# Kernel optimization log

Hardware: AMD Instinct MI355X
Metric: run time of the kernel (lower is better)

Reference implementation:

```python
import jax, jax.numpy as jnp
import numpy as np

B, S, E, H = 4, 2048, 1024, 16
D = E // H  # d_k = 64
NEG = -1000000000.0  # matches torch masked_fill constant


def setup_inputs() -> dict:
    rk = jax.random.key(0)
    kq, kk, kv, km = jax.random.split(rk, 4)
    query = jax.random.normal(kq, (B, S, E), dtype=jnp.float32)
    key = jax.random.normal(kk, (B, S, E), dtype=jnp.float32)
    value = jax.random.normal(kv, (B, S, E), dtype=jnp.float32)
    mask = jax.random.randint(km, (B, S, S), 0, 2, dtype=jnp.int32)
    return {"query": query, "key": key, "value": value, "mask": mask}


def _split_heads(x):
    # (B, S, E) -> (B, H, S, D)
    return x.reshape(B, S, H, D).transpose(0, 2, 1, 3)


def reference(query, key, value, mask):
    q = _split_heads(query)
    k = _split_heads(key)
    v = _split_heads(value)
    scale = np.float32(1.0 / np.sqrt(D))
    scores = jnp.einsum('bhqd,bhkd->bhqk', q, k) * scale  # (B,H,S,S)
    scores = jnp.where(mask[:, None, :, :] == 0, jnp.float32(NEG), scores)
    weights = jax.nn.softmax(scores, axis=-1)
    attn = jnp.einsum('bhqk,bhkd->bhqd', weights, v)  # (B,H,S,D)
    concat = attn.transpose(0, 2, 1, 3).reshape(B, S, E)
    return concat
```

## Files before the change

kernel.cpp:

```cpp
#include <hip/hip_runtime.h>
#include <hip/hip_bf16.h>
#include <math.h>

constexpr int B = 4, S = 2048, E = 1024, H = 16, D = 64;
constexpr float NEGF = -1000000000.0f;
constexpr float KSCALE = 0.125f * 1.44269504f;

typedef __attribute__((ext_vector_type(8))) short short8;
typedef __attribute__((ext_vector_type(16))) float f32x16;

__device__ inline unsigned pk2(float a, float b) {
    unsigned ua = __builtin_bit_cast(unsigned, a) + 0x8000u;
    unsigned ub = __builtin_bit_cast(unsigned, b) + 0x8000u;
    return __builtin_amdgcn_perm(ub, ua, 0x07060302u);
}
__device__ inline void gl_lds16(const void* g, void* l) {
    __builtin_amdgcn_global_load_lds(
        (const __attribute__((address_space(1))) unsigned int*)g,
        (__attribute__((address_space(3))) unsigned int*)l, 16, 0, 0);
}

constexpr size_t WS_K  = 0;
constexpr size_t WS_VT = 18874368;
constexpr size_t WS_MB = 37748736;
constexpr size_t WS_NEED = 54525952;

__global__ void prep_all(const float* __restrict__ K, const float* __restrict__ V,
                         const int* __restrict__ M, char* __restrict__ ws) {
    __shared__ float Vf[64][69];
    const int bid = blockIdx.x, tid = threadIdx.x;

    {
        int g = bid * 256 + tid;
        int rowd = g >> 2, qtr = g & 3;
        int b = rowd >> 15, h = (rowd >> 11) & 15, s = rowd & 2047;
        const float* p = K + ((size_t)(b * S + s)) * E + h * 64 + qtr * 16;
        float4 v0 = *(const float4*)(p + 0),  v1 = *(const float4*)(p + 4);
        float4 v2 = *(const float4*)(p + 8),  v3 = *(const float4*)(p + 12);
        uint4 o0, o1;
        o0.x = pk2(v0.x * KSCALE, v0.y * KSCALE); o0.y = pk2(v0.z * KSCALE, v0.w * KSCALE);
        o0.z = pk2(v1.x * KSCALE, v1.y * KSCALE); o0.w = pk2(v1.z * KSCALE, v1.w * KSCALE);
        o1.x = pk2(v2.x * KSCALE, v2.y * KSCALE); o1.y = pk2(v2.z * KSCALE, v2.w * KSCALE);
        o1.z = pk2(v3.x * KSCALE, v3.y * KSCALE); o1.w = pk2(v3.z * KSCALE, v3.w * KSCALE);
        char* d = ws + WS_K + (size_t)rowd * 144 + qtr * 32;
        *(uint4*)d = o0; *(uint4*)(d + 16) = o1;
        if (qtr == 3) {
            uint4 z; z.x = z.y = z.z = z.w = 0;
            *(uint4*)(d + 32) = z;
        }
    }

    {
        int bh = bid >> 5, kt = bid & 31;
        int b = bh >> 4, h = bh & 15;
        {
            int r = tid >> 2, c4 = (tid & 3) * 16;
            const float* p = V + ((size_t)(b * S + kt * 64 + r)) * E + h * 64 + c4;
            float4 a = *(const float4*)(p + 0), bb = *(const float4*)(p + 4);
            float4 c = *(const float4*)(p + 8), dd = *(const float4*)(p + 12);
            *(float4*)&Vf[r][c4 + 0] = a;  *(float4*)&Vf[r][c4 + 4] = bb;
            *(float4*)&Vf[r][c4 + 8] = c;  *(float4*)&Vf[r][c4 + 12] = dd;
        }
        __syncthreads();
        int d = tid >> 2, sq = (tid & 3) * 16;
        float v[16];
#pragma unroll
        for (int i = 0; i < 16; ++i) v[i] = Vf[sq + i][d];
        uint4 o0, o1;
        o0.x = pk2(v[0], v[1]);   o0.y = pk2(v[2], v[3]);
        o0.z = pk2(v[4], v[5]);   o0.w = pk2(v[6], v[7]);
        o1.x = pk2(v[8], v[9]);   o1.y = pk2(v[10], v[11]);
        o1.z = pk2(v[12], v[13]); o1.w = pk2(v[14], v[15]);
        char* o = ws + WS_VT + ((size_t)(bh * 32 + kt)) * 9216 + d * 144 + sq * 2;
        *(uint4*)o = o0; *(uint4*)(o + 16) = o1;
        if (sq == 48) {
            uint4 z; z.x = z.y = z.z = z.w = 0;
            *(uint4*)(o + 32) = z;
        }
    }

    {
        unsigned* Mb = (unsigned*)(ws + WS_MB);
        const int t = bid * 256 + tid;
#pragma unroll
        for (int it = 0; it < 8; ++it) {
            int gidx = it * 524288 + t;
            int4 mv = *((const int4*)M + gidx);
            unsigned d = (mv.x ? 0xFFu : 0u) | (mv.y ? 0xFF00u : 0u)
                       | (mv.z ? 0xFF0000u : 0u) | (mv.w ? 0xFF000000u : 0u);
            int row = gidx >> 4, g = gidx & 15;
            Mb[row * 16 + (g & 1) * 8 + (g >> 1)] = d;
        }
    }
}

__global__ __launch_bounds__(256, 2)
void fa_mfma(const float* __restrict__ Q, const char* __restrict__ ws,
             float* __restrict__ O) {
    __shared__ char smem[55296];
    const int tid = threadIdx.x;
    const int w = tid >> 6, lane = tid & 63;
    const int L5 = lane & 31, h6 = lane >> 5;
    const int h = blockIdx.x & 15, b = (blockIdx.x >> 4) & 3, qt = blockIdx.x >> 6;
    const int bh = b * 16 + h;
    const int q0w = qt * 256 + w * 64;
    char* const Ps = smem + 18432 + w * 9216;

    const char* Kws  = ws + WS_K;
    const char* Vtws = ws + WS_VT;
    const int qA = q0w + L5, qB = qA + 32;
    const char* mrowA = ws + WS_MB + ((size_t)(b * S + qA)) * 2048 + h6 * 32;
    const char* mrowB = ws + WS_MB + ((size_t)(b * S + qB)) * 2048 + h6 * 32;

    short8 qf[2][4];
#pragma unroll
    for (int nb = 0; nb < 2; ++nb)
#pragma unroll
        for (int ks = 0; ks < 4; ++ks) {
            const float* qp = Q + ((size_t)(b * S + q0w + nb * 32 + L5)) * E
                                + h * 64 + ks * 16 + h6 * 8;
            float4 a = *(const float4*)qp;
            float4 c = *(const float4*)(qp + 4);
            uint4 u;
            u.x = pk2(a.x, a.y); u.y = pk2(a.z, a.w);
            u.z = pk2(c.x, c.y); u.w = pk2(c.z, c.w);
            qf[nb][ks] = *(short8*)&u;
        }

    f32x16 acc[2][2];
#pragma unroll
    for (int mb = 0; mb < 2; ++mb)
#pragma unroll
        for (int nb = 0; nb < 2; ++nb) acc[mb][nb] = (f32x16)0.0f;
    float l0 = 0.0f, l1 = 0.0f;

    for (int ti = 0; ti < 32; ++ti) {
        const uint4 mAl = *(const uint4*)(mrowA + ti * 64);
        const uint4 mAh = *(const uint4*)(mrowA + ti * 64 + 16);
        const uint4 mBl = *(const uint4*)(mrowB + ti * 64);
        const uint4 mBh = *(const uint4*)(mrowB + ti * 64 + 16);
        const unsigned mdwA[8] = {mAl.x, mAl.y, mAl.z, mAl.w, mAh.x, mAh.y, mAh.z, mAh.w};
        const unsigned mdwB[8] = {mBl.x, mBl.y, mBl.z, mBl.w, mBh.x, mBh.y, mBh.z, mBh.w};

        __syncthreads();
        {
            const char* ksrc = Kws + ((size_t)bh * S + ti * 64) * 144;
            const char* vsrc = Vtws + ((size_t)(bh * 32 + ti)) * 9216;
#pragma unroll
            for (int c = 0; c < 5; ++c) {
                int idx = c * 4 + w;
                if (idx < 18) {
                    int off = idx * 1024;
                    const char* g = (off < 9216) ? (ksrc + off) : (vsrc + off - 9216);
                    gl_lds16(g + lane * 16, smem + off);
                }
            }
        }
        __syncthreads();

#pragma unroll
        for (int mbK = 0; mbK < 2; ++mbK) {
            short8 kf[4];
#pragma unroll
            for (int ks = 0; ks < 4; ++ks)
                kf[ks] = *(const short8*)(smem + (mbK * 32 + L5) * 144 + ks * 32 + h6 * 16);
#pragma unroll
            for (int nb = 0; nb < 2; ++nb) {
                f32x16 s = (f32x16)0.0f;
#pragma unroll
                for (int ks = 0; ks < 4; ++ks)
                    s = __builtin_amdgcn_mfma_f32_32x32x16_bf16(kf[ks], qf[nb][ks], s, 0, 0, 0);

                const unsigned* mdw = nb ? mdwB : mdwA;
                float lacc = 0.0f;
                unsigned pd[8];
#pragma unroll
                for (int i = 0; i < 8; ++i) {
                    float e0 = __builtin_amdgcn_exp2f(s[2 * i]);
                    float e1 = __builtin_amdgcn_exp2f(s[2 * i + 1]);
                    unsigned pm = pk2(e0, e1);
                    const unsigned mv = mdw[mbK * 4 + (i >> 1)];
                    const unsigned am = __builtin_amdgcn_perm(
                        mv, mv, (i & 1) ? 0x03030202u : 0x01010000u);
                    pm &= am;
                    pd[i] = pm;
                    float lo = __builtin_bit_cast(float, pm << 16);
                    float hi = __builtin_bit_cast(float, pm & 0xFFFF0000u);
                    lacc += lo + hi;
                }
                if (nb) l1 += lacc; else l0 += lacc;

                char* prow = Ps + (nb * 32 + L5) * 144 + mbK * 64 + h6 * 8;
#pragma unroll
                for (int g4 = 0; g4 < 4; ++g4) {
                    uint2 t; t.x = pd[2 * g4]; t.y = pd[2 * g4 + 1];
                    *(uint2*)(prow + g4 * 16) = t;
                }
            }
        }

        __builtin_amdgcn_s_waitcnt(0xc07f);

        short8 pf[2][4];
#pragma unroll
        for (int nb = 0; nb < 2; ++nb)
#pragma unroll
            for (int ks = 0; ks < 4; ++ks)
                pf[nb][ks] = *(const short8*)(Ps + (nb * 32 + L5) * 144 + ks * 32 + h6 * 16);
#pragma unroll
        for (int mbV = 0; mbV < 2; ++mbV) {
            short8 vf[4];
#pragma unroll
            for (int ks = 0; ks < 4; ++ks)
                vf[ks] = *(const short8*)(smem + 9216 + (mbV * 32 + L5) * 144 + ks * 32 + h6 * 16);
#pragma unroll
            for (int nb = 0; nb < 2; ++nb)
#pragma unroll
                for (int ks = 0; ks < 4; ++ks)
                    acc[mbV][nb] = __builtin_amdgcn_mfma_f32_32x32x16_bf16(
                        vf[ks], pf[nb][ks], acc[mbV][nb], 0, 0, 0);
        }
    }

    l0 += __shfl_xor(l0, 32, 64);
    l1 += __shfl_xor(l1, 32, 64);
    const float inv[2] = {1.0f / l0, 1.0f / l1};
    __syncthreads();
#pragma unroll
    for (int nb = 0; nb < 2; ++nb) {
#pragma unroll
        for (int mb = 0; mb < 2; ++mb)
#pragma unroll
            for (int g4 = 0; g4 < 4; ++g4) {
                float4 t;
                t.x = acc[mb][nb][g4 * 4 + 0] * inv[nb];
                t.y = acc[mb][nb][g4 * 4 + 1] * inv[nb];
                t.z = acc[mb][nb][g4 * 4 + 2] * inv[nb];
                t.w = acc[mb][nb][g4 * 4 + 3] * inv[nb];
                *(float4*)(Ps + (L5 * 68 + mb * 32 + g4 * 8 + h6 * 4) * 4) = t;
            }
        __builtin_amdgcn_s_waitcnt(0xc07f);
        const int r16 = lane >> 4, dc = lane & 15;
#pragma unroll
        for (int i = 0; i < 8; ++i) {
            const int row = i * 4 + r16;
            float4 t = *(const float4*)(Ps + (row * 68 + dc * 4) * 4);
            *(float4*)(O + ((size_t)b * S + q0w + nb * 32 + row) * E + h * 64 + dc * 4) = t;
        }
        __builtin_amdgcn_s_waitcnt(0xc07f);
    }
}

constexpr int QT = 64, KT = 64, LD = D + 4;
constexpr float SCALE = 0.125f;
__global__ __launch_bounds__(256, 3)
void fa_fp32(const float* __restrict__ Q, const float* __restrict__ K,
             const float* __restrict__ V, const int* __restrict__ M,
             float* __restrict__ Out)
{
    __shared__ float Qs[QT][LD];
    __shared__ float Vs[KT][LD];
    __shared__ float KPs[KT][LD];
    const int tid = threadIdx.x, tx = tid & 15, ty = tid >> 4;
    const int bid = blockIdx.x;
    const int h = bid % H, b = (bid / H) % B, qt = bid / (H * B);
    const int q0 = qt * QT;
    {
        const int col = tx * 4;
#pragma unroll
        for (int i = 0; i < 4; ++i) {
            const int row = ty + i * 16;
            *(float4*)&Qs[row][col] = *(const float4*)&Q[((size_t)(b * S + q0 + row)) * E + h * D + col];
        }
    }
    const int qr0 = ty * 4, d0 = tx * 4;
    float acc[4][4] = {};
    float m_i[4], l_i[4];
#pragma unroll
    for (int j = 0; j < 4; ++j) { m_i[j] = -INFINITY; l_i[j] = 0.0f; }
    for (int kt = 0; kt < S; kt += KT) {
        __syncthreads();
        {
            const int col = tx * 4;
#pragma unroll
            for (int i = 0; i < 4; ++i) {
                const int row = ty + i * 16;
                const size_t g = ((size_t)(b * S + kt + row)) * E + h * D + col;
                *(float4*)&KPs[row][col] = *(const float4*)&K[g];
                *(float4*)&Vs[row][col] = *(const float4*)&V[g];
            }
        }
        __syncthreads();
        float s[4][4] = {};
#pragma unroll
        for (int d = 0; d < D; d += 4) {
            float4 a[4], bb[4];
#pragma unroll
            for (int j = 0; j < 4; ++j) a[j] = *(const float4*)&Qs[qr0 + j][d];
#pragma unroll
            for (int i = 0; i < 4; ++i) bb[i] = *(const float4*)&KPs[tx + 16 * i][d];
#pragma unroll
            for (int j = 0; j < 4; ++j)
#pragma unroll
                for (int i = 0; i < 4; ++i)
                    s[j][i] += a[j].x * bb[i].x + a[j].y * bb[i].y + a[j].z * bb[i].z + a[j].w * bb[i].w;
        }
#pragma unroll
        for (int j = 0; j < 4; ++j) {
            const int* mrow = &M[((size_t)b * S + (q0 + qr0 + j)) * S + kt];
#pragma unroll
            for (int i = 0; i < 4; ++i) {
                const int mk = mrow[tx + 16 * i];
                s[j][i] = mk ? s[j][i] * SCALE : NEGF;
            }
        }
#pragma unroll
        for (int j = 0; j < 4; ++j) {
            float tm = fmaxf(fmaxf(s[j][0], s[j][1]), fmaxf(s[j][2], s[j][3]));
#pragma unroll
            for (int off = 8; off; off >>= 1) tm = fmaxf(tm, __shfl_xor(tm, off, 16));
            const float nm = fmaxf(m_i[j], tm);
            const float alpha = __expf(m_i[j] - nm);
            m_i[j] = nm;
            float rs = 0.0f;
#pragma unroll
            for (int i = 0; i < 4; ++i) { const float p = __expf(s[j][i] - nm); s[j][i] = p; rs += p; }
#pragma unroll
            for (int off = 8; off; off >>= 1) rs += __shfl_xor(rs, off, 16);
            l_i[j] = l_i[j] * alpha + rs;
#pragma unroll
            for (int dd = 0; dd < 4; ++dd) acc[j][dd] *= alpha;
        }
        __syncthreads();
#pragma unroll
        for (int j = 0; j < 4; ++j)
#pragma unroll
            for (int i = 0; i < 4; ++i) KPs[qr0 + j][tx + 16 * i] = s[j][i];
        __syncthreads();
#pragma unroll 4
        for (int kk = 0; kk < KT; kk += 4) {
            float4 p[4], vv[4];
#pragma unroll
            for (int j = 0; j < 4; ++j) p[j] = *(const float4*)&KPs[qr0 + j][kk];
#pragma unroll
            for (int u = 0; u < 4; ++u) vv[u] = *(const float4*)&Vs[kk + u][d0];
#pragma unroll
            for (int j = 0; j < 4; ++j) {
                acc[j][0] += p[j].x * vv[0].x + p[j].y * vv[1].x + p[j].z * vv[2].x + p[j].w * vv[3].x;
                acc[j][1] += p[j].x * vv[0].y + p[j].y * vv[1].y + p[j].z * vv[2].y + p[j].w * vv[3].y;
                acc[j][2] += p[j].x * vv[0].z + p[j].y * vv[1].z + p[j].z * vv[2].z + p[j].w * vv[3].z;
                acc[j][3] += p[j].x * vv[0].w + p[j].y * vv[1].w + p[j].z * vv[2].w + p[j].w * vv[3].w;
            }
        }
    }
#pragma unroll
    for (int j = 0; j < 4; ++j) {
        const float iv = 1.0f / l_i[j];
        float4 r;
        r.x = acc[j][0] * iv; r.y = acc[j][1] * iv; r.z = acc[j][2] * iv; r.w = acc[j][3] * iv;
        *(float4*)&Out[((size_t)(b * S + q0 + qr0 + j)) * E + h * D + d0] = r;
    }
}

extern "C" void kernel_launch(void* const* d_in, const int* in_sizes, int n_in,
                              void* d_out, int out_size, void* d_ws, size_t ws_size,
                              hipStream_t stream) {
    (void)in_sizes; (void)n_in; (void)out_size;
    const float* q = (const float*)d_in[0];
    const float* k = (const float*)d_in[1];
    const float* v = (const float*)d_in[2];
    const int*   m = (const int*)d_in[3];
    float* out = (float*)d_out;

    if (ws_size >= WS_NEED) {
        char* ws = (char*)d_ws;
        prep_all<<<2048, 256, 0, stream>>>(k, v, m, ws);
        fa_mfma<<<512, 256, 0, stream>>>(q, ws, out);
    } else {
        fa_fp32<<<B * H * (S / QT), 256, 0, stream>>>(q, k, v, m, out);
    }
}
```

Baseline: 288.6 us.

## Double-buffer K/V tiles and keep P in registers via permlane32 swap

The K/V tile loads into LDS are now double-buffered: the next tile is prefetched while the current one is computed, with one barrier per iteration instead of two. The softmax probabilities no longer round-trip through per-wave LDS scratch. They are rearranged into MFMA B-operand layout in registers with v_permlane32_swap, and the PV MFMAs are interleaved per key half-block. The smaller LDS footprint allows three blocks per CU, and s_setprio is placed around the MFMA groups. Risks include higher register pressure under the tighter launch bound, and correctness depends on the permlane swap matching the fragment layout. The global_load_lds prefetch also relies on the end-of-iteration barrier for visibility, with no explicit vmcnt wait.

After: 436.7 us. 1.51x slower.

```diff
diff --git a/kernel.cpp b/kernel.cpp
--- a/kernel.cpp
+++ b/kernel.cpp
@@ -18,6 +18,9 @@
     __builtin_amdgcn_global_load_lds(
         (const __attribute__((address_space(1))) unsigned int*)g,
         (__attribute__((address_space(3))) unsigned int*)l, 16, 0, 0);
+}
+__device__ inline void plswap(unsigned& a, unsigned& b) {
+    asm volatile("v_permlane32_swap_b32 %0, %1" : "+v"(a), "+v"(b));
 }
 
 constexpr size_t WS_K  = 0;
@@ -94,20 +97,19 @@
     }
 }
 
-__global__ __launch_bounds__(256, 2)
+__global__ __launch_bounds__(256, 3)
 void fa_mfma(const float* __restrict__ Q, const char* __restrict__ ws,
              float* __restrict__ O) {
-    __shared__ char smem[55296];
+    __shared__ char smem[36864];
     const int tid = threadIdx.x;
     const int w = tid >> 6, lane = tid & 63;
     const int L5 = lane & 31, h6 = lane >> 5;
     const int h = blockIdx.x & 15, b = (blockIdx.x >> 4) & 3, qt = blockIdx.x >> 6;
     const int bh = b * 16 + h;
     const int q0w = qt * 256 + w * 64;
-    char* const Ps = smem + 18432 + w * 9216;
-
-    const char* Kws  = ws + WS_K;
-    const char* Vtws = ws + WS_VT;
+
+    const char* const ksrc_bh = ws + WS_K + (size_t)bh * S * 144;
+    const char* const vsrc_bh = ws + WS_VT + (size_t)bh * 32 * 9216;
     const int qA = q0w + L5, qB = qA + 32;
     const char* mrowA = ws + WS_MB + ((size_t)(b * S + qA)) * 2048 + h6 * 32;
     const char* mrowB = ws + WS_MB + ((size_t)(b * S + qB)) * 2048 + h6 * 32;
@@ -134,42 +136,63 @@
         for (int nb = 0; nb < 2; ++nb) acc[mb][nb] = (f32x16)0.0f;
     float l0 = 0.0f, l1 = 0.0f;
 
+    {
+#pragma unroll
+        for (int c = 0; c < 5; ++c) {
+            int idx = c * 4 + w;
+            if (idx < 18) {
+                int off = idx * 1024;
+                const char* g = (off < 9216) ? (ksrc_bh + off) : (vsrc_bh + off - 9216);
+                gl_lds16(g + lane * 16, smem + off);
+            }
+        }
+    }
+    __syncthreads();
+
     for (int ti = 0; ti < 32; ++ti) {
+        char* const buf = smem + (ti & 1) * 18432;
+
         const uint4 mAl = *(const uint4*)(mrowA + ti * 64);
         const uint4 mAh = *(const uint4*)(mrowA + ti * 64 + 16);
         const uint4 mBl = *(const uint4*)(mrowB + ti * 64);
         const uint4 mBh = *(const uint4*)(mrowB + ti * 64 + 16);
         const unsigned mdwA[8] = {mAl.x, mAl.y, mAl.z, mAl.w, mAh.x, mAh.y, mAh.z, mAh.w};
         const unsigned mdwB[8] = {mBl.x, mBl.y, mBl.z, mBl.w, mBh.x, mBh.y, mBh.z, mBh.w};
-
-        __syncthreads();
-        {
-            const char* ksrc = Kws + ((size_t)bh * S + ti * 64) * 144;
-            const char* vsrc = Vtws + ((size_t)(bh * 32 + ti)) * 9216;
+        __builtin_amdgcn_sched_barrier(0);
+
+        if (ti < 31) {
+            char* const nbuf = smem + ((ti + 1) & 1) * 18432;
+            const char* ksrc = ksrc_bh + (size_t)(ti + 1) * 9216;
+            const char* vsrc = vsrc_bh + (size_t)(ti + 1) * 9216;
 #pragma unroll
             for (int c = 0; c < 5; ++c) {
                 int idx = c * 4 + w;
                 if (idx < 18) {
                     int off = idx * 1024;
                     const char* g = (off < 9216) ? (ksrc + off) : (vsrc + off - 9216);
-                    gl_lds16(g + lane * 16, smem + off);
+                    gl_lds16(g + lane * 16, nbuf + off);
                 }
             }
         }
-        __syncthreads();
+
+        const char* bufK = buf;
+        const char* bufV = buf + 9216;
 
 #pragma unroll
         for (int mbK = 0; mbK < 2; ++mbK) {
             short8 kf[4];
 #pragma unroll
             for (int ks = 0; ks < 4; ++ks)
-                kf[ks] = *(const short8*)(smem + (mbK * 32 + L5) * 144 + ks * 32 + h6 * 16);
+                kf[ks] = *(const short8*)(bufK + (mbK * 32 + L5) * 144 + ks * 32 + h6 * 16);
+            short8 pf[2][2];
 #pragma unroll
             for (int nb = 0; nb < 2; ++nb) {
                 f32x16 s = (f32x16)0.0f;
+                __builtin_amdgcn_s_setprio(1);
 #pragma unroll
                 for (int ks = 0; ks < 4; ++ks)
                     s = __builtin_amdgcn_mfma_f32_32x32x16_bf16(kf[ks], qf[nb][ks], s, 0, 0, 0);
+                __builtin_amdgcn_s_setprio(0);
 
                 const unsigned* mdw = nb ? mdwB : mdwA;
                 float lacc = 0.0f;
@@ -190,42 +213,38 @@
                 }
                 if (nb) l1 += lacc; else l0 += lacc;
 
-                char* prow = Ps + (nb * 32 + L5) * 144 + mbK * 64 + h6 * 8;
-#pragma unroll
-                for (int g4 = 0; g4 < 4; ++g4) {
-                    uint2 t; t.x = pd[2 * g4]; t.y = pd[2 * g4 + 1];
-                    *(uint2*)(prow + g4 * 16) = t;
-                }
-            }
-        }
-
-        __builtin_amdgcn_s_waitcnt(0xc07f);
-
-        short8 pf[2][4];
-#pragma unroll
-        for (int nb = 0; nb < 2; ++nb)
-#pragma unroll
-            for (int ks = 0; ks < 4; ++ks)
-                pf[nb][ks] = *(const short8*)(Ps + (nb * 32 + L5) * 144 + ks * 32 + h6 * 16);
-#pragma unroll
-        for (int mbV = 0; mbV < 2; ++mbV) {
-            short8 vf[4];
-#pragma unroll
-            for (int ks = 0; ks < 4; ++ks)
-                vf[ks] = *(const short8*)(smem + 9216 + (mbV * 32 + L5) * 144 + ks * 32 + h6 * 16);
-#pragma unroll
-            for (int nb = 0; nb < 2; ++nb)
-#pragma unroll
-                for (int ks = 0; ks < 4; ++ks)
-                    acc[mbV][nb] = __builtin_amdgcn_mfma_f32_32x32x16_bf16(
-                        vf[ks], pf[nb][ks], acc[mbV][nb], 0, 0, 0);
-        }
-    }
-
+                plswap(pd[0], pd[2]); plswap(pd[1], pd[3]);
+                plswap(pd[4], pd[6]); plswap(pd[5], pd[7]);
+                uint4 f0; f0.x = pd[0]; f0.y = pd[1]; f0.z = pd[2]; f0.w = pd[3];
+                uint4 f1; f1.x = pd[4]; f1.y = pd[5]; f1.z = pd[6]; f1.w = pd[7];
+                pf[nb][0] = *(short8*)&f0;
+                pf[nb][1] = *(short8*)&f1;
+            }
+
+#pragma unroll
+            for (int mbV = 0; mbV < 2; ++mbV) {
+                short8 vf[2];
+#pragma unroll
+                for (int s2 = 0; s2 < 2; ++s2)
+                    vf[s2] = *(const short8*)(bufV + (mbV * 32 + L5) * 144
+                                              + (mbK * 2 + s2) * 32 + h6 * 16);
+                __builtin_amdgcn_s_setprio(1);
+#pragma unroll
+                for (int nb = 0; nb < 2; ++nb)
+#pragma unroll
+                    for (int s2 = 0; s2 < 2; ++s2)
+                        acc[mbV][nb] = __builtin_amdgcn_mfma_f32_32x32x16_bf16(
+                            vf[s2], pf[nb][s2], acc[mbV][nb], 0, 0, 0);
+                __builtin_amdgcn_s_setprio(0);
+            }
+        }
+        __syncthreads();
+    }
+
+    char* const Pse = smem + w * 8704;
     l0 += __shfl_xor(l0, 32, 64);
     l1 += __shfl_xor(l1, 32, 64);
     const float inv[2] = {1.0f / l0, 1.0f / l1};
-    __syncthreads();
 #pragma unroll
     for (int nb = 0; nb < 2; ++nb) {
 #pragma unroll
@@ -237,14 +256,14 @@
                 t.y = acc[mb][nb][g4 * 4 + 1] * inv[nb];
                 t.z = acc[mb][nb][g4 * 4 + 2] * inv[nb];
                 t.w = acc[mb][nb][g4 * 4 + 3] * inv[nb];
-                *(float4*)(Ps + (L5 * 68 + mb * 32 + g4 * 8 + h6 * 4) * 4) = t;
+                *(float4*)(Pse + (L5 * 68 + mb * 32 + g4 * 8 + h6 * 4) * 4) = t;
             }
         __builtin_amdgcn_s_waitcnt(0xc07f);
         const int r16 = lane >> 4, dc = lane & 15;
 #pragma unroll
         for (int i = 0; i < 8; ++i) {
             const int row = i * 4 + r16;
-            float4 t = *(const float4*)(Ps + (row * 68 + dc * 4) * 4);
+            float4 t = *(const float4*)(Pse + (row * 68 + dc * 4) * 4);
             *(float4*)(O + ((size_t)b * S + q0w + nb * 32 + row) * E + h * 64 + dc * 4) = t;
         }
         __builtin_amdgcn_s_waitcnt(0xc07f);
```
